# Performance work log

Measured on AMD Instinct MI355X. Metric: run time of the kernel, lower is better.

Reference implementation:

```python
import jax, jax.numpy as jnp
import numpy as np

V, DM, CD, K, CH, B, T, NC = 32000, 128, 32, 8, 4, 64, 2048, 8
LAM, RHO, LR = 0.05, 0.9, 0.03
FEAT = DM + CD + DM + DM + 2  # 418


def ln(x, w, b, eps=1e-5):
    m = x.mean(-1, keepdims=True)
    v = ((x - m) ** 2).mean(-1, keepdims=True)
    return (x - m) * jax.lax.rsqrt(v + eps) * w + b


def l2norm(x, axis):
    n = jnp.sqrt(jnp.sum(x * x, axis=axis, keepdims=True))
    return x / jnp.maximum(n, 1e-12)


def topk_shrink(x, lam, k):
    s = jnp.sign(x) * jax.nn.relu(jnp.abs(x) - lam)
    _, idx = jax.lax.top_k(jnp.abs(s), k)                      # [B,k]
    mask = jnp.any(jax.nn.one_hot(idx, s.shape[-1], dtype=bool), axis=-2)
    return jnp.where(mask, s, 0.0)


def conv1d(x, w, b, pad):
    # x [B,T,Cin], w [k,Cin,Cout]
    y = jax.lax.conv_general_dilated(x, w, (1,), ((pad, pad),),
                                     dimension_numbers=("NWC", "WIO", "NWC"))
    return y + b


def glu(x):
    a, g = jnp.split(x, 2, axis=-1)
    return a * jax.nn.sigmoid(g)


def forward(tokens, emb, in_w, in_b, c1w, c1b, c2w, c2b, op_w, op_b, on_w, on_b,
            base_D, wcu, wcc, wcdu, bcdu, wcdc, bcdc, wg, bg,
            un_w, un_b, cn_w, cn_b, cl_w, cl_b, f1w, f1b, f2w, f2b):
    token_mask = tokens != 0
    # ---- local phrase encoder ----
    x = emb[tokens]                                            # [B,T,DM]
    x = ln(x, in_w, in_b)
    y1 = glu(conv1d(x, c1w, c1b, 1))                           # [B,T,DM]
    y2 = glu(conv1d(x, c2w, c2b, 2))                           # [B,T,DM]
    y = jnp.concatenate([y1, y2], -1) @ op_w + op_b            # [B,T,DM]
    h = ln(x + y, on_w, on_b)
    # ---- surface pooling ----
    mf = token_mask.astype(h.dtype)[..., None]
    denom = jnp.maximum(mf.sum(1), 1.0)
    surface_mean = (h * mf).sum(1) / denom                     # [B,DM]
    neg = jnp.finfo(h.dtype).min
    smax = jnp.where(token_mask[..., None], h, neg).max(axis=1)
    fully = ~token_mask.any(axis=1)
    surface_max = jnp.where(fully[:, None], 0.0, smax)
    # ---- chunk mean pool ----
    chunks = T // CH
    hc = h.reshape(B, chunks, CH, DM)
    mc = token_mask.reshape(B, chunks, CH)
    mcf = mc.astype(h.dtype)
    den = jnp.maximum(mcf.sum(2, keepdims=True), 1.0)
    chunk_h = (hc * mcf[..., None]).sum(2) / den               # [B,chunks,DM]
    chunk_mask = mc.any(2)                                     # [B,chunks]
    # ---- sparse semantic field scan ----
    D0 = l2norm(jnp.broadcast_to(base_D, (B, DM, CD)), axis=1)
    c0 = jnp.zeros((B, CD), h.dtype)

    def step(carry, inp):
        D, c_prev = carry
        u, valid = inp                                         # u [B,DM], valid [B,1]
        logits = ln(u, un_w, un_b) @ wcu + ln(c_prev, cn_w, cn_b) @ wcc
        a = topk_shrink(logits, LAM, K)                        # [B,CD]
        u_hat = jnp.einsum('bdc,bc->bd', D, a)
        r = u - u_hat
        c_new = RHO * c_prev + (1.0 - RHO) * a
        c_t = valid * c_new + (1.0 - valid) * c_prev
        d_local = l2norm(D + LR * r[:, :, None] * a[:, None, :], axis=1)
        err = jnp.sqrt(jnp.sum(r * r, -1, keepdims=True))      # [B,1]
        gate = jax.nn.sigmoid(jnp.concatenate([u, c_t, err], -1) @ wg + bg)
        cand = (u @ wcdu + bcdu) + (c_t @ wcdc + bcdc)
        d_cand = l2norm(cand.reshape(B, DM, CD), axis=1)
        g = gate[:, :, None]
        d_next = l2norm((1.0 - g) * d_local + g * d_cand, axis=1)
        v = valid[:, :, None]
        d_next = v * d_next + (1.0 - v) * D
        z = jnp.einsum('bdc,bc->bd', d_next, c_t)
        return (d_next, c_t), (z, err, gate)

    xs = (chunk_h.transpose(1, 0, 2), chunk_mask.T.astype(h.dtype)[..., None])
    (Dn, c_last), (zs, errs, gates) = jax.lax.scan(step, (D0, c0), xs)
    feat = jnp.concatenate([zs[-1], c_last, surface_mean, surface_max,
                            errs[-1], gates[-1]], -1)          # [B,FEAT]
    feat = ln(feat, cl_w, cl_b)
    hcls = jax.nn.gelu(feat @ f1w + f1b, approximate=False)
    return hcls @ f2w + f2b                                    # [B,NC]


def setup_inputs() -> dict:
    ks = iter(jax.random.split(jax.random.key(0), 64))
    rn = lambda shape, s=0.02: jax.random.normal(next(ks), shape, jnp.float32) * s
    tokens = jax.random.randint(next(ks), (B, T), 0, V)
    return {
        'tokens': tokens,
        'emb': rn((V, DM)).at[0].set(0.0),
        'in_w': jnp.ones((DM,)), 'in_b': jnp.zeros((DM,)),
        'c1w': rn((3, DM, 2 * DM)), 'c1b': jnp.zeros((2 * DM,)),
        'c2w': rn((5, DM, 2 * DM)), 'c2b': jnp.zeros((2 * DM,)),
        'op_w': rn((2 * DM, DM)), 'op_b': jnp.zeros((DM,)),
        'on_w': jnp.ones((DM,)), 'on_b': jnp.zeros((DM,)),
        'base_D': rn((DM, CD)),
        'wcu': rn((DM, CD), 0.05), 'wcc': rn((CD, CD), 0.05),
        'wcdu': rn((DM, DM * CD)), 'bcdu': jnp.zeros((DM * CD,)),
        'wcdc': rn((CD, DM * CD)), 'bcdc': jnp.zeros((DM * CD,)),
        'wg': rn((DM + CD + 1, 1)), 'bg': jnp.zeros((1,)),
        'un_w': jnp.ones((DM,)), 'un_b': jnp.zeros((DM,)),
        'cn_w': jnp.ones((CD,)), 'cn_b': jnp.zeros((CD,)),
        'cl_w': jnp.ones((FEAT,)), 'cl_b': jnp.zeros((FEAT,)),
        'f1w': rn((FEAT, 2 * DM)), 'f1b': jnp.zeros((2 * DM,)),
        'f2w': rn((2 * DM, NC)), 'f2b': jnp.zeros((NC,)),
    }


def reference(tokens, emb, in_w, in_b, c1w, c1b, c2w, c2b, op_w, op_b, on_w, on_b,
              base_D, wcu, wcc, wcdu, bcdu, wcdc, bcdc, wg, bg,
              un_w, un_b, cn_w, cn_b, cl_w, cl_b, f1w, f1b, f2w, f2b):
    return forward(tokens, emb, in_w, in_b, c1w, c1b, c2w, c2b, op_w, op_b,
                   on_w, on_b, base_D, wcu, wcc, wcdu, bcdu, wcdc, bcdc, wg, bg,
                   un_w, un_b, cn_w, cn_b, cl_w, cl_b, f1w, f1b, f2w, f2b)
```

## Files before the change

### kernel.cpp

```cpp
#include <hip/hip_runtime.h>
#include <hip/hip_bf16.h>
#include <cfloat>
#include <cstdio>

#define TT   2048
#define BB   64
#define DMD  128
#define CDD  32
#define NCH  512
#define FEATN 418
#define LDW  33
#define APITCH 132
#define YPITCH 257

#define WOFF2(kc,c) ((kc)*144 + (c)*8 + (((c)>>2)<<2))

__device__ __forceinline__ float redx16(float v) {
  v += __shfl_xor(v, 1); v += __shfl_xor(v, 2);
  v += __shfl_xor(v, 4); v += __shfl_xor(v, 8);
  return v;
}
__device__ __forceinline__ float redx32(float v) { v = redx16(v); v += __shfl_xor(v, 16); return v; }
__device__ __forceinline__ float redx64(float v) { v = redx32(v); v += __shfl_xor(v, 32); return v; }
__device__ __forceinline__ float bfbits2f(unsigned int u) {
  union { unsigned int i; float f; } v; v.i = u << 16; return v.f;
}
__device__ __forceinline__ unsigned short f2bf(float f) {
  union { float f; unsigned int i; } u; u.f = f;
  unsigned int r = u.i + 0x7FFFu + ((u.i >> 16) & 1u);
  return (unsigned short)(r >> 16);
}
__device__ __forceinline__ float sigmoidf_(float x) { return 1.f / (1.f + expf(-x)); }

__device__ __forceinline__ void load_cand8(const unsigned short* cand, size_t idx, float* pf) {
  uint4 v = *reinterpret_cast<const uint4*>(cand + idx);
  pf[0] = bfbits2f(v.x & 0xFFFFu); pf[1] = bfbits2f(v.x >> 16);
  pf[2] = bfbits2f(v.y & 0xFFFFu); pf[3] = bfbits2f(v.y >> 16);
  pf[4] = bfbits2f(v.z & 0xFFFFu); pf[5] = bfbits2f(v.z >> 16);
  pf[6] = bfbits2f(v.w & 0xFFFFu); pf[7] = bfbits2f(v.w >> 16);
}

typedef __attribute__((ext_vector_type(8))) short s8v;
typedef __attribute__((ext_vector_type(4))) float f4v;
union F8 { s8v v; unsigned short u[8]; uint4 q; };

__global__ __launch_bounds__(256) void k_prep_conv(
    const float* __restrict__ c1w, const float* __restrict__ c2w,
    unsigned short* __restrict__ W3hi, unsigned short* __restrict__ W3lo,
    unsigned short* __restrict__ W5hi, unsigned short* __restrict__ W5lo) {
  int tid = blockIdx.x * 256 + threadIdx.x;
  const float* src; unsigned short *dh, *dl; int fid;
  if (tid < 12288) { fid = tid;        src = c1w; dh = W3hi; dl = W3lo; }
  else             { fid = tid - 12288; src = c2w; dh = W5hi; dl = W5lo; }
  int lane = fid & 63;
  int nt   = (fid >> 6) & 15;
  int kc   = (fid >> 10) & 3;
  int tap  = fid >> 12;
  int col  = nt * 16 + (lane & 15);
  int kb   = tap * 128 + kc * 32 + (lane >> 4) * 8;
  F8 hi, lo;
  #pragma unroll
  for (int j = 0; j < 8; ++j) {
    float wv = src[(size_t)(kb + j) * 256 + col];
    unsigned short h = f2bf(wv);
    hi.u[j] = h;
    lo.u[j] = f2bf(wv - bfbits2f(h));
  }
  *reinterpret_cast<uint4*>(dh + (size_t)fid * 8) = hi.q;
  *reinterpret_cast<uint4*>(dl + (size_t)fid * 8) = lo.q;
}

__global__ __launch_bounds__(256) void k_front(
    const int* __restrict__ tokens, const float* __restrict__ emb,
    const float* __restrict__ inw, const float* __restrict__ inb,
    const unsigned short* __restrict__ W3hi, const unsigned short* __restrict__ W3lo,
    const unsigned short* __restrict__ W5hi, const unsigned short* __restrict__ W5lo,
    const float* __restrict__ c1b, const float* __restrict__ c2b,
    const float* __restrict__ opw, const float* __restrict__ opb,
    const float* __restrict__ onw, const float* __restrict__ onb,
    const float* __restrict__ unw, const float* __restrict__ unb,
    const float* __restrict__ wcu, const float* __restrict__ wgv,
    float* __restrict__ chunk_h, float* __restrict__ validf,
    float* __restrict__ lgu, float* __restrict__ gu,
    float* __restrict__ spsum, float* __restrict__ spmax, float* __restrict__ spcnt) {
  __shared__ float A[36 * APITCH];
  __shared__ float Y[32 * YPITCH];
  __shared__ float ABf[4608];
  __shared__ float tokm[32];
  unsigned short* Ahi = (unsigned short*)ABf;
  unsigned short* Alo = Ahi + 36 * 128;
  const int b = blockIdx.y, tile = blockIdx.x;
  const int t0 = tile * 32;
  const int t = threadIdx.x;
  const int lane = t & 63, wq = t >> 6;

  for (int r = wq; r < 36; r += 4) {
    int p = t0 + r - 2;
    float2 o = make_float2(0.f, 0.f);
    if (p >= 0 && p < TT) {
      int tok = tokens[b * TT + p];
      if (lane == 0 && r >= 2 && r < 34) tokm[r - 2] = (tok != 0) ? 1.f : 0.f;
      float2 e = *reinterpret_cast<const float2*>(emb + (size_t)tok * DMD + lane * 2);
      float mean = redx64(e.x + e.y) * (1.f / 128.f);
      float d0 = e.x - mean, d1 = e.y - mean;
      float vvv = redx64(d0 * d0 + d1 * d1) * (1.f / 128.f);
      float rs = rsqrtf(vvv + 1e-5f);
      o.x = d0 * rs * inw[lane * 2]     + inb[lane * 2];
      o.y = d1 * rs * inw[lane * 2 + 1] + inb[lane * 2 + 1];
    }
    *reinterpret_cast<float2*>(&A[r * APITCH + lane * 2]) = o;
    unsigned short hx = f2bf(o.x), hy = f2bf(o.y);
    unsigned short lx = f2bf(o.x - bfbits2f(hx)), ly = f2bf(o.y - bfbits2f(hy));
    int slot = (lane >> 2) ^ (r & 7);
    int ui = r * 64 + slot * 4 + (lane & 3);
    ((unsigned int*)Ahi)[ui] = (unsigned int)hx | ((unsigned int)hy << 16);
    ((unsigned int*)Alo)[ui] = (unsigned int)lx | ((unsigned int)ly << 16);
  }
  __syncthreads();

  const int l16 = lane & 15, lk = lane >> 4;
  f4v acc3[2][4], acc5[2][4];
  #pragma unroll
  for (int mt = 0; mt < 2; ++mt)
    #pragma unroll
    for (int nf = 0; nf < 4; ++nf) { acc3[mt][nf] = (f4v)(0.f); acc5[mt][nf] = (f4v)(0.f); }
  #pragma unroll
  for (int d = 0; d < 5; ++d) {
    #pragma unroll
    for (int kc = 0; kc < 4; ++kc) {
      F8 ahi[2], alo[2];
      #pragma unroll
      for (int mt = 0; mt < 2; ++mt) {
        int arow = mt * 16 + l16 + d;
        int s = (kc * 4 + lk) ^ (arow & 7);
        ahi[mt].q = *reinterpret_cast<const uint4*>(Ahi + arow * 128 + s * 8);
        alo[mt].q = *reinterpret_cast<const uint4*>(Alo + arow * 128 + s * 8);
      }
      #pragma unroll
      for (int nf = 0; nf < 4; ++nf) {
        int nt = (nf < 2) ? (wq * 2 + nf) : (8 + wq * 2 + nf - 2);
        size_t off = ((size_t)((d * 4 + kc) * 16 + nt) * 64 + lane) * 8;
        F8 bh, bl;
        bh.q = *reinterpret_cast<const uint4*>(W5hi + off);
        bl.q = *reinterpret_cast<const uint4*>(W5lo + off);
        #pragma unroll
        for (int mt = 0; mt < 2; ++mt) {
          acc5[mt][nf] = __builtin_amdgcn_mfma_f32_16x16x32_bf16(ahi[mt].v, bh.v, acc5[mt][nf], 0, 0, 0);
          acc5[mt][nf] = __builtin_amdgcn_mfma_f32_16x16x32_bf16(ahi[mt].v, bl.v, acc5[mt][nf], 0, 0, 0);
          acc5[mt][nf] = __builtin_amdgcn_mfma_f32_16x16x32_bf16(alo[mt].v, bh.v, acc5[mt][nf], 0, 0, 0);
          acc5[mt][nf] = __builtin_amdgcn_mfma_f32_16x16x32_bf16(alo[mt].v, bl.v, acc5[mt][nf], 0, 0, 0);
        }
      }
      if (d >= 1 && d <= 3) {
        int tap = d - 1;
        #pragma unroll
        for (int nf = 0; nf < 4; ++nf) {
          int nt = (nf < 2) ? (wq * 2 + nf) : (8 + wq * 2 + nf - 2);
          size_t off = ((size_t)((tap * 4 + kc) * 16 + nt) * 64 + lane) * 8;
          F8 bh, bl;
          bh.q = *reinterpret_cast<const uint4*>(W3hi + off);
          bl.q = *reinterpret_cast<const uint4*>(W3lo + off);
          #pragma unroll
          for (int mt = 0; mt < 2; ++mt) {
            acc3[mt][nf] = __builtin_amdgcn_mfma_f32_16x16x32_bf16(ahi[mt].v, bh.v, acc3[mt][nf], 0, 0, 0);
            acc3[mt][nf] = __builtin_amdgcn_mfma_f32_16x16x32_bf16(ahi[mt].v, bl.v, acc3[mt][nf], 0, 0, 0);
            acc3[mt][nf] = __builtin_amdgcn_mfma_f32_16x16x32_bf16(alo[mt].v, bh.v, acc3[mt][nf], 0, 0, 0);
            acc3[mt][nf] = __builtin_amdgcn_mfma_f32_16x16x32_bf16(alo[mt].v, bl.v, acc3[mt][nf], 0, 0, 0);
          }
        }
      }
    }
  }
  #pragma unroll
  for (int mt = 0; mt < 2; ++mt)
    #pragma unroll
    for (int nf = 0; nf < 2; ++nf) {
      int col = wq * 32 + nf * 16 + l16;
      #pragma unroll
      for (int r = 0; r < 4; ++r) {
        int row = mt * 16 + lk * 4 + r;
        float av3 = acc3[mt][nf][r]     + c1b[col];
        float gv3 = acc3[mt][nf + 2][r] + c1b[128 + col];
        Y[row * YPITCH + col] = av3 * sigmoidf_(gv3);
        float av5 = acc5[mt][nf][r]     + c2b[col];
        float gv5 = acc5[mt][nf + 2][r] + c2b[128 + col];
        Y[row * YPITCH + 128 + col] = av5 * sigmoidf_(gv5);
      }
    }
  __syncthreads();

  const int tm = t >> 4, tn = t & 15;
  const int r0 = tm * 2;
  float* Wl = ABf;
  float acc2[2][8] = {};
  {
    const int kcw = t >> 4, cw2 = t & 15;
    {
      float4 wr0 = *reinterpret_cast<const float4*>(&opw[(size_t)kcw * 128 + cw2 * 8]);
      float4 wr1 = *reinterpret_cast<const float4*>(&opw[(size_t)kcw * 128 + cw2 * 8 + 4]);
      *reinterpret_cast<float4*>(&Wl[WOFF2(kcw, cw2)])     = wr0;
      *reinterpret_cast<float4*>(&Wl[WOFF2(kcw, cw2) + 4]) = wr1;
    }
    __syncthreads();
    for (int k0 = 0; k0 < 256; k0 += 16) {
      float* Wb = Wl + (((k0 >> 4) & 1) ? 2304 : 0);
      const bool more = (k0 + 16) < 256;
      float4 nr0, nr1;
      if (more) {
        nr0 = *reinterpret_cast<const float4*>(&opw[(size_t)(k0 + 16 + kcw) * 128 + cw2 * 8]);
        nr1 = *reinterpret_cast<const float4*>(&opw[(size_t)(k0 + 16 + kcw) * 128 + cw2 * 8 + 4]);
      }
      #pragma unroll
      for (int kc = 0; kc < 16; ++kc) {
        int k = k0 + kc;
        float y0 = Y[r0 * YPITCH + k];
        float y1 = Y[(r0 + 1) * YPITCH + k];
        float w8[8];
        *reinterpret_cast<float4*>(&w8[0]) = *reinterpret_cast<float4*>(&Wb[WOFF2(kc, tn)]);
        *reinterpret_cast<float4*>(&w8[4]) = *reinterpret_cast<float4*>(&Wb[WOFF2(kc, tn) + 4]);
        #pragma unroll
        for (int q = 0; q < 8; ++q) { acc2[0][q] += y0 * w8[q]; acc2[1][q] += y1 * w8[q]; }
      }
      if (more) {
        float* Wn = Wl + ((((k0 >> 4) + 1) & 1) ? 2304 : 0);
        *reinterpret_cast<float4*>(&Wn[WOFF2(kcw, cw2)])     = nr0;
        *reinterpret_cast<float4*>(&Wn[WOFF2(kcw, cw2) + 4]) = nr1;
      }
      __syncthreads();
    }
  }

  const int col = tn * 8;
  float hreg[2][8];
  float msk[2];
  #pragma unroll
  for (int m = 0; m < 2; ++m) {
    int row = r0 + m;
    float vals[8]; float s = 0.f;
    const float* xr = &A[(row + 2) * APITCH + col];
    #pragma unroll
    for (int q = 0; q < 8; ++q) { vals[q] = acc2[m][q] + opb[col + q] + xr[q]; s += vals[q]; }
    s = redx16(s);
    float mean = s * (1.f / 128.f);
    float vv2 = 0.f;
    #pragma unroll
    for (int q = 0; q < 8; ++q) { float d = vals[q] - mean; vv2 += d * d; }
    vv2 = redx16(vv2) * (1.f / 128.f);
    float rs = rsqrtf(vv2 + 1e-5f);
    #pragma unroll
    for (int q = 0; q < 8; ++q) hreg[m][q] = (vals[q] - mean) * rs * onw[col + q] + onb[col + q];
    msk[m] = tokm[row];
  }

  __syncthreads();
  float* partS = Y;
  float* partM = Y + 2048;
  float* lnus  = Y + 4096;
  float ps[8], pm[8];
  #pragma unroll
  for (int q = 0; q < 8; ++q) {
    ps[q] = msk[0] * hreg[0][q] + msk[1] * hreg[1][q];
    float m0 = (msk[0] != 0.f) ? hreg[0][q] : -FLT_MAX;
    float m1 = (msk[1] != 0.f) ? hreg[1][q] : -FLT_MAX;
    pm[q] = fmaxf(m0, m1);
  }
  #pragma unroll
  for (int q = 0; q < 8; ++q) { partS[tm * 128 + col + q] = ps[q]; partM[tm * 128 + col + q] = pm[q]; }

  float ccnt = msk[0] + msk[1];
  float csum[8];
  #pragma unroll
  for (int q = 0; q < 8; ++q) csum[q] = ps[q];
  #pragma unroll
  for (int q = 0; q < 8; ++q) csum[q] += __shfl_xor(csum[q], 16);
  ccnt += __shfl_xor(ccnt, 16);

  if ((tm & 1) == 0) {
    int jg = tile * 8 + (tm >> 1);
    float inv = 1.f / fmaxf(ccnt, 1.f);
    float cm[8];
    #pragma unroll
    for (int q = 0; q < 8; ++q) cm[q] = csum[q] * inv;
    *reinterpret_cast<float4*>(&chunk_h[((size_t)b * NCH + jg) * DMD + col])     = *reinterpret_cast<float4*>(&cm[0]);
    *reinterpret_cast<float4*>(&chunk_h[((size_t)b * NCH + jg) * DMD + col + 4]) = *reinterpret_cast<float4*>(&cm[4]);
    if (tn == 0) validf[jg * BB + b] = (ccnt > 0.f) ? 1.f : 0.f;
    float gp = 0.f;
    #pragma unroll
    for (int q = 0; q < 8; ++q) gp += cm[q] * wgv[col + q];
    gp = redx16(gp);
    if (tn == 0) gu[(size_t)jg * BB + b] = gp;
    float s2 = 0.f;
    #pragma unroll
    for (int q = 0; q < 8; ++q) s2 += cm[q];
    s2 = redx16(s2);
    float mean2 = s2 * (1.f / 128.f);
    float v3 = 0.f;
    #pragma unroll
    for (int q = 0; q < 8; ++q) { float d = cm[q] - mean2; v3 += d * d; }
    v3 = redx16(v3) * (1.f / 128.f);
    float rs2 = rsqrtf(v3 + 1e-5f);
    int ch = tm >> 1;
    #pragma unroll
    for (int q = 0; q < 8; ++q) lnus[ch * 128 + col + q] = (cm[q] - mean2) * rs2 * unw[col + q] + unb[col + q];
  }
  __syncthreads();
  {
    int ch = t >> 5, o = t & 31;
    float accl = 0.f;
    for (int d = 0; d < 128; ++d) accl += lnus[ch * 128 + d] * wcu[d * 32 + o];
    int jg2 = tile * 8 + ch;
    lgu[((size_t)jg2 * BB + b) * 32 + o] = accl;
  }
  if (t < 128) {
    float s3 = 0.f, m3 = -FLT_MAX;
    #pragma unroll
    for (int g = 0; g < 16; ++g) { s3 += partS[g * 128 + t]; m3 = fmaxf(m3, partM[g * 128 + t]); }
    spsum[((size_t)b * 64 + tile) * DMD + t] = s3;
    spmax[((size_t)b * 64 + tile) * DMD + t] = m3;
  }
  if (t == 128) {
    float cnt = 0.f;
    for (int r = 0; r < 32; ++r) cnt += tokm[r];
    spcnt[b * 64 + tile] = cnt;
  }
}

__global__ __launch_bounds__(128) void k_surface(
    const float* __restrict__ spsum, const float* __restrict__ spmax, const float* __restrict__ spcnt,
    float* __restrict__ smean, float* __restrict__ smax) {
  const int b = blockIdx.x, d = threadIdx.x;
  float s = 0.f, m = -FLT_MAX, cnt = 0.f;
  for (int p = 0; p < 64; ++p) {
    s += spsum[((size_t)b * 64 + p) * DMD + d];
    m = fmaxf(m, spmax[((size_t)b * 64 + p) * DMD + d]);
    cnt += spcnt[b * 64 + p];
  }
  smean[b * DMD + d] = s / fmaxf(cnt, 1.f);
  smax[b * DMD + d] = (cnt > 0.f) ? m : 0.f;
}

__global__ __launch_bounds__(256) void k_prep_w(
    const float* __restrict__ wcdu, const float* __restrict__ wcdc,
    unsigned short* __restrict__ Whi, unsigned short* __restrict__ Wlo) {
  int tid = blockIdx.x * 256 + threadIdx.x;
  int lane = tid & 63;
  int ks = (tid >> 6) % 5;
  int nt = tid / 320;
  int col = nt * 16 + (lane & 15);
  int kbase = ks * 32 + (lane >> 4) * 8;
  F8 hi, lo;
  #pragma unroll
  for (int j = 0; j < 8; ++j) {
    int k = kbase + j;
    float wv = (k < 128) ? wcdu[(size_t)k * 4096 + col] : wcdc[(size_t)(k - 128) * 4096 + col];
    unsigned short h = f2bf(wv);
    hi.u[j] = h;
    lo.u[j] = f2bf(wv - bfbits2f(h));
  }
  *reinterpret_cast<uint4*>(Whi + (size_t)tid * 8) = hi.q;
  *reinterpret_cast<uint4*>(Wlo + (size_t)tid * 8) = lo.q;
}

__global__ __launch_bounds__(256) void k_cand_mfma(
    const float* __restrict__ chunk_h, const float* __restrict__ c_g,
    const unsigned short* __restrict__ Whi, const unsigned short* __restrict__ Wlo,
    const float* __restrict__ bcdu, const float* __restrict__ bcdc,
    unsigned short* __restrict__ cand, int j0) {
  const int lj = blockIdx.y, j = j0 + lj;
  const int w = threadIdx.x >> 6, l = threadIdx.x & 63;
  const int nb = blockIdx.x * 256 + w * 64;
  const int l16 = l & 15, lk = l >> 4;
  f4v acc[4][4];
  #pragma unroll
  for (int mf = 0; mf < 4; ++mf)
    #pragma unroll
    for (int nf = 0; nf < 4; ++nf) acc[mf][nf] = (f4v)(0.f);
  #pragma unroll
  for (int ks = 0; ks < 5; ++ks) {
    F8 ahi[4], alo[4];
    #pragma unroll
    for (int mf = 0; mf < 4; ++mf) {
      int row = mf * 16 + l16;
      float av[8];
      if (ks < 4) {
        const float* src = chunk_h + ((size_t)row * NCH + j) * DMD + ks * 32 + lk * 8;
        *reinterpret_cast<float4*>(&av[0]) = *reinterpret_cast<const float4*>(src);
        *reinterpret_cast<float4*>(&av[4]) = *reinterpret_cast<const float4*>(src + 4);
      } else {
        const float* src = c_g + ((size_t)j * BB + row) * 32 + lk * 8;
        *reinterpret_cast<float4*>(&av[0]) = *reinterpret_cast<const float4*>(src);
        *reinterpret_cast<float4*>(&av[4]) = *reinterpret_cast<const float4*>(src + 4);
      }
      #pragma unroll
      for (int q = 0; q < 8; ++q) {
        unsigned short h = f2bf(av[q]);
        ahi[mf].u[q] = h;
        alo[mf].u[q] = f2bf(av[q] - bfbits2f(h));
      }
    }
    #pragma unroll
    for (int nf = 0; nf < 4; ++nf) {
      int nt = (nb >> 4) + nf;
      size_t off = (((size_t)nt * 5 + ks) * 64 + l) * 8;
      F8 bhi, blo;
      bhi.q = *reinterpret_cast<const uint4*>(Whi + off);
      blo.q = *reinterpret_cast<const uint4*>(Wlo + off);
      #pragma unroll
      for (int mf = 0; mf < 4; ++mf) {
        acc[mf][nf] = __builtin_amdgcn_mfma_f32_16x16x32_bf16(ahi[mf].v, bhi.v, acc[mf][nf], 0, 0, 0);
        acc[mf][nf] = __builtin_amdgcn_mfma_f32_16x16x32_bf16(ahi[mf].v, blo.v, acc[mf][nf], 0, 0, 0);
        acc[mf][nf] = __builtin_amdgcn_mfma_f32_16x16x32_bf16(alo[mf].v, bhi.v, acc[mf][nf], 0, 0, 0);
      }
    }
  }
  #pragma unroll
  for (int nf = 0; nf < 4; ++nf) {
    int colc = nb + nf * 16 + l16;
    float bias = bcdu[colc] + bcdc[colc];
    #pragma unroll
    for (int mf = 0; mf < 4; ++mf) {
      #pragma unroll
      for (int r = 0; r < 4; ++r) {
        int row = mf * 16 + lk * 4 + r;
        cand[((size_t)lj * BB + row) * 4096 + colc] = f2bf(acc[mf][nf][r] + bias);
      }
    }
  }
}

__global__ __launch_bounds__(64) void k_accrec(
    const float* __restrict__ lgu, const float* __restrict__ gu,
    const float* __restrict__ validf,
    const float* __restrict__ wcc, const float* __restrict__ cnw, const float* __restrict__ cnb,
    const float* __restrict__ wg, const float* __restrict__ bg,
    float* __restrict__ a_g, float* __restrict__ c_g, float* __restrict__ gpart_g) {
  __shared__ float wcc_l[CDD * CDD];
  __shared__ float cn_s[CDD];
  __shared__ float as_s[CDD];
  const int t = threadIdx.x, l = t & 31;
  const int b = blockIdx.x;
  for (int i = t; i < CDD * CDD; i += 64) wcc_l[i] = wcc[i];
  __syncthreads();
  const float cw = cnw[l], cb = cnb[l], wgc = wg[DMD + l];
  const float bgs = bg[0];
  float c = 0.f;
  float lg = lgu[(size_t)b * 32 + l];
  float vld = validf[b];
  float guv = gu[b];
  for (int j = 0; j < NCH; ++j) {
    const int jn = (j + 1 < NCH) ? j + 1 : j;
    const size_t jbn = (size_t)jn * BB + b;
    float lgN = lgu[jbn * 32 + l];
    float vldN = validf[jbn];
    float guvN = gu[jbn];
    float mean = redx32(c) * (1.f / 32.f);
    float dv = c - mean;
    float var = redx32(dv * dv) * (1.f / 32.f);
    float cn = dv * rsqrtf(var + 1e-5f) * cw + cb;
    if (t < 32) cn_s[l] = cn;
    float l0 = lg, l1 = 0.f;
    #pragma unroll
    for (int i = 0; i < 16; ++i) {
      l0 += cn_s[i] * wcc_l[i * 32 + l];
      l1 += cn_s[i + 16] * wcc_l[(i + 16) * 32 + l];
    }
    float logit = l0 + l1;
    float sv = (logit > 0.05f) ? (logit - 0.05f) : ((logit < -0.05f) ? (logit + 0.05f) : 0.f);
    float as = fabsf(sv);
    if (t < 32) as_s[l] = as;
    int r0 = 0, r1 = 0;
    #pragma unroll
    for (int i = 0; i < 16; ++i) {
      float a0 = as_s[i], a1 = as_s[i + 16];
      r0 += (a0 > as || (a0 == as && i < l)) ? 1 : 0;
      r1 += (a1 > as || (a1 == as && (i + 16) < l)) ? 1 : 0;
    }
    float av = ((r0 + r1) < 8) ? sv : 0.f;
    float ct = (vld != 0.f) ? (0.9f * c + 0.1f * av) : c;
    c = ct;
    float dotc = redx32(ct * wgc);
    if (t < 32) {
      const size_t jb = (size_t)j * BB + b;
      a_g[jb * 32 + l] = av;
      c_g[jb * 32 + l] = ct;
      if (l == 0) gpart_g[jb] = guv + dotc + bgs;
    }
    lg = lgN; vld = vldN; guv = guvN;
  }
}

__global__ __launch_bounds__(512) void k_scan_seg(
    const float* __restrict__ chunk_h, const float* __restrict__ a_gg,
    const float* __restrict__ c_g, const float* __restrict__ gpart_g,
    const float* __restrict__ validf,
    const unsigned short* __restrict__ cand, int j0, int slen,
    const float* __restrict__ wg, const float* __restrict__ base_D,
    float* __restrict__ Dst,
    const float* __restrict__ smean, const float* __restrict__ smax,
    const float* __restrict__ clw, const float* __restrict__ clb,
    const float* __restrict__ f1w, const float* __restrict__ f1b,
    const float* __restrict__ f2w, const float* __restrict__ f2b,
    float* __restrict__ out) {
  __shared__ float Dl[DMD * LDW];
  __shared__ float Cl[DMD * LDW];
  __shared__ float a_l[CDD];
  __shared__ float r_l[DMD];
  __shared__ float red[8];
  __shared__ float feat[FEATN + 2];
  __shared__ float featn[FEATN + 2];
  __shared__ float h1[256];

  const int b = blockIdx.x;
  const int t = threadIdx.x;
  const int c = t >> 4;
  const int rg = t & 15;
  const bool doInit = (j0 == 0);
  const bool doHead = (j0 + slen >= NCH);
  const float wge = wg[160];

  if (doInit) {
    for (int i = t; i < DMD * CDD; i += 512) Dl[(i >> 5) * LDW + (i & 31)] = base_D[i];
  } else {
    for (int i = t; i < DMD * CDD; i += 512) Dl[(i >> 5) * LDW + (i & 31)] = Dst[(size_t)b * 4096 + i];
  }
  __syncthreads();
  float Dv[8];
  if (doInit) {
    float s = 0.f;
    #pragma unroll
    for (int m = 0; m < 8; ++m) { Dv[m] = Dl[(rg + 16 * m) * LDW + c]; s += Dv[m] * Dv[m]; }
    s = redx16(s);
    float inv = 1.f / fmaxf(sqrtf(s), 1e-12f);
    #pragma unroll
    for (int m = 0; m < 8; ++m) { Dv[m] *= inv; Dl[(rg + 16 * m) * LDW + c] = Dv[m]; }
  } else {
    #pragma unroll
    for (int m = 0; m < 8; ++m) Dv[m] = Dl[(rg + 16 * m) * LDW + c];
  }
  float pf[8];
  load_cand8(cand, ((size_t)0 * BB + b) * 4096 + (size_t)t * 8, pf);
  float un_r = (t < DMD) ? chunk_h[((size_t)b * NCH + j0) * DMD + t] : 0.f;
  float a_col = a_gg[((size_t)j0 * BB + b) * 32 + c];
  if (t < 32) a_l[t] = a_gg[((size_t)j0 * BB + b) * 32 + t];
  float gpart = gpart_g[(size_t)j0 * BB + b];
  float vld = validf[(size_t)j0 * BB + b];
  float err = 0.f, gate = 0.f;

  for (int lj = 0; lj < slen; ++lj) {
    __syncthreads();
    {
      int dd = t >> 2, cc0 = (t & 3) * 8;
      #pragma unroll
      for (int q = 0; q < 8; ++q) Cl[dd * LDW + cc0 + q] = pf[q];
    }
    if (t < DMD) {
      float uh = 0.f;
      #pragma unroll
      for (int cc = 0; cc < 32; ++cc) uh += a_l[cc] * Dl[t * LDW + cc];
      float rr = un_r - uh;
      r_l[t] = rr;
      float rp = redx64(rr * rr);
      if ((t & 63) == 0) red[t >> 6] = rp;
    }
    __syncthreads();
    err = sqrtf(red[0] + red[1]);
    gate = sigmoidf_(gpart + err * wge);
    const int ljn = (lj + 1 < slen) ? (lj + 1) : lj;
    const int jn = j0 + ljn;
    float pfN[8];
    load_cand8(cand, ((size_t)ljn * BB + b) * 4096 + (size_t)t * 8, pfN);
    float unN = (t < DMD) ? chunk_h[((size_t)b * NCH + jn) * DMD + t] : 0.f;
    float aColN = a_gg[((size_t)jn * BB + b) * 32 + c];
    float a32N = (t < 32) ? a_gg[((size_t)jn * BB + b) * 32 + t] : 0.f;
    float gpN = gpart_g[(size_t)jn * BB + b];
    float vldN = validf[(size_t)jn * BB + b];
    float dl[8], dcv[8], dn[8];
    float sl = 0.f, sc = 0.f;
    #pragma unroll
    for (int m = 0; m < 8; ++m) {
      int e = (rg + 16 * m) * LDW + c;
      dl[m] = Dv[m] + 0.03f * r_l[rg + 16 * m] * a_col;
      sl += dl[m] * dl[m];
      dcv[m] = Cl[e];
      sc += dcv[m] * dcv[m];
    }
    sl = redx16(sl); sc = redx16(sc);
    float il = 1.f / fmaxf(sqrtf(sl), 1e-12f);
    float ic = 1.f / fmaxf(sqrtf(sc), 1e-12f);
    float g1 = 1.f - gate;
    float sn = 0.f;
    #pragma unroll
    for (int m = 0; m < 8; ++m) { dn[m] = g1 * dl[m] * il + gate * dcv[m] * ic; sn += dn[m] * dn[m]; }
    sn = redx16(sn);
    float inn = 1.f / fmaxf(sqrtf(sn), 1e-12f);
    const bool vb = (vld != 0.f);
    #pragma unroll
    for (int m = 0; m < 8; ++m) {
      if (vb) Dv[m] = dn[m] * inn;
      Dl[(rg + 16 * m) * LDW + c] = Dv[m];
    }
    if (t < 32) a_l[t] = a32N;
    #pragma unroll
    for (int q = 0; q < 8; ++q) pf[q] = pfN[q];
    un_r = unN; a_col = aColN; gpart = gpN; vld = vldN;
  }
  __syncthreads();
  for (int i = t; i < 4096; i += 512) Dst[(size_t)b * 4096 + i] = Dl[(i >> 5) * LDW + (i & 31)];
  if (!doHead) return;
  if (t < 32) a_l[t] = c_g[((size_t)(NCH - 1) * BB + b) * 32 + t];
  __syncthreads();
  if (t < DMD) {
    float z = 0.f;
    #pragma unroll
    for (int cc = 0; cc < 32; ++cc) z += Dl[t * LDW + cc] * a_l[cc];
    feat[t] = z;
    feat[160 + t] = smean[b * DMD + t];
    feat[288 + t] = smax[b * DMD + t];
  }
  if (t >= 128 && t < 160) feat[t] = a_l[t - 128];
  if (t == 0) { feat[416] = err; feat[417] = gate; }
  __syncthreads();
  float fv = (t < FEATN) ? feat[t] : 0.f;
  float ws1 = redx64(fv);
  if ((t & 63) == 0) red[t >> 6] = ws1;
  __syncthreads();
  float tot = 0.f;
  #pragma unroll
  for (int w = 0; w < 8; ++w) tot += red[w];
  float mean = tot * (1.f / 418.f);
  float dvv = (t < FEATN) ? (fv - mean) : 0.f;
  float ws2 = redx64(dvv * dvv);
  __syncthreads();
  if ((t & 63) == 0) red[t >> 6] = ws2;
  __syncthreads();
  float vtot = 0.f;
  #pragma unroll
  for (int w = 0; w < 8; ++w) vtot += red[w];
  float rs = rsqrtf(vtot * (1.f / 418.f) + 1e-5f);
  if (t < FEATN) featn[t] = (fv - mean) * rs * clw[t] + clb[t];
  __syncthreads();
  if (t < 256) {
    float acc = f1b[t];
    for (int f = 0; f < FEATN; ++f) acc += featn[f] * f1w[(size_t)f * 256 + t];
    h1[t] = acc * 0.5f * (1.f + erff(acc * 0.70710678f));
  }
  __syncthreads();
  if (t < 8) {
    float acc = f2b[t];
    #pragma unroll 8
    for (int i = 0; i < 256; ++i) acc += h1[i] * f2w[i * 8 + t];
    out[b * 8 + t] = acc;
  }
}

extern "C" void kernel_launch(void* const* d_in, const int* in_sizes, int n_in,
                              void* d_out, int out_size, void* d_ws, size_t ws_size,
                              hipStream_t stream) {
  const int*   tokens = (const int*)d_in[0];
  const float* emb    = (const float*)d_in[1];
  const float* in_w   = (const float*)d_in[2];
  const float* in_b   = (const float*)d_in[3];
  const float* c1w    = (const float*)d_in[4];
  const float* c1b    = (const float*)d_in[5];
  const float* c2w    = (const float*)d_in[6];
  const float* c2b    = (const float*)d_in[7];
  const float* op_w   = (const float*)d_in[8];
  const float* op_b   = (const float*)d_in[9];
  const float* on_w   = (const float*)d_in[10];
  const float* on_b   = (const float*)d_in[11];
  const float* base_D = (const float*)d_in[12];
  const float* wcu    = (const float*)d_in[13];
  const float* wcc    = (const float*)d_in[14];
  const float* wcdu   = (const float*)d_in[15];
  const float* bcdu   = (const float*)d_in[16];
  const float* wcdc   = (const float*)d_in[17];
  const float* bcdc   = (const float*)d_in[18];
  const float* wg     = (const float*)d_in[19];
  const float* bg     = (const float*)d_in[20];
  const float* un_w   = (const float*)d_in[21];
  const float* un_b   = (const float*)d_in[22];
  const float* cn_w   = (const float*)d_in[23];
  const float* cn_b   = (const float*)d_in[24];
  const float* cl_w   = (const float*)d_in[25];
  const float* cl_b   = (const float*)d_in[26];
  const float* f1w    = (const float*)d_in[27];
  const float* f1b    = (const float*)d_in[28];
  const float* f2w    = (const float*)d_in[29];
  const float* f2b    = (const float*)d_in[30];

  const size_t CHEL = (size_t)BB * NCH * DMD;
  const size_t NB   = (size_t)NCH * BB;
  size_t fixedFloats = CHEL + NB + NB * 32 + NB
                     + (size_t)BB * 64 * DMD * 2 + (size_t)BB * 64
                     + (size_t)BB * DMD * 2 + (size_t)BB * 4096
                     + NB * 32 + NB * 32 + NB;
  const size_t WFRAG  = 655360ull;
  const size_t W3FR   = 98304ull;
  const size_t W5FR   = 163840ull;
  const size_t WSWZ_BYTES = (2ull * WFRAG + 2ull * W3FR + 2ull * W5FR) * 2ull;
  const size_t FIXED_BYTES = fixedFloats * 4 + WSWZ_BYTES;
  const size_t SEG_UNIT = (size_t)BB * 4096 * 2;
  int S = 512;
  while (S > 1 && (size_t)S * SEG_UNIT + FIXED_BYTES > ws_size) S >>= 1;

  unsigned short* cand = (unsigned short*)d_ws;
  unsigned short* Whi  = (unsigned short*)((char*)d_ws + (size_t)S * SEG_UNIT);
  unsigned short* Wlo  = Whi + WFRAG;
  unsigned short* W3hi = Wlo + WFRAG;
  unsigned short* W3lo = W3hi + W3FR;
  unsigned short* W5hi = W3lo + W3FR;
  unsigned short* W5lo = W5hi + W5FR;
  float* base = (float*)(W5lo + W5FR);
  float* chunk_h = base; base += CHEL;
  float* validf  = base; base += NB;
  float* lgu     = base; base += NB * 32;
  float* gu      = base; base += NB;
  float* spsum   = base; base += (size_t)BB * 64 * DMD;
  float* spmax   = base; base += (size_t)BB * 64 * DMD;
  float* spcnt   = base; base += (size_t)BB * 64;
  float* smean   = base; base += (size_t)BB * DMD;
  float* smaxv   = base; base += (size_t)BB * DMD;
  float* Dst     = base; base += (size_t)BB * 4096;
  float* a_g     = base; base += NB * 32;
  float* c_g     = base; base += NB * 32;
  float* gpart   = base; base += NB;
  float* out = (float*)d_out;
  fprintf(stderr, "[hsfc69] ws_size=%zu fixed=%zu S=%d total=%zu\n",
          ws_size, FIXED_BYTES, S, FIXED_BYTES + (size_t)S * SEG_UNIT);

  k_prep_w<<<dim3(320), dim3(256), 0, stream>>>(wcdu, wcdc, Whi, Wlo);
  k_prep_conv<<<dim3(128), dim3(256), 0, stream>>>(c1w, c2w, W3hi, W3lo, W5hi, W5lo);
  k_front<<<dim3(64, BB), dim3(256), 0, stream>>>(
      tokens, emb, in_w, in_b, W3hi, W3lo, W5hi, W5lo, c1b, c2b,
      op_w, op_b, on_w, on_b, un_w, un_b, wcu, wg,
      chunk_h, validf, lgu, gu, spsum, spmax, spcnt);
  k_surface<<<dim3(BB), dim3(128), 0, stream>>>(spsum, spmax, spcnt, smean, smaxv);
  k_accrec<<<dim3(BB), dim3(64), 0, stream>>>(
      lgu, gu, validf, wcc, cn_w, cn_b, wg, bg, a_g, c_g, gpart);
  for (int j0 = 0; j0 < NCH; j0 += S) {
    k_cand_mfma<<<dim3(16, S), dim3(256), 0, stream>>>(
        chunk_h, c_g, Whi, Wlo, bcdu, bcdc, cand, j0);
    k_scan_seg<<<dim3(BB), dim3(512), 0, stream>>>(
        chunk_h, a_g, c_g, gpart, validf, cand, j0, S,
        wg, base_D, Dst, smean, smaxv, cl_w, cl_b, f1w, f1b, f2w, f2b, out);
  }
}
```

Before: 2.995 ms.

## Store candidate dictionaries column-major so scan threads read own columns directly

```diff
diff --git a/kernel.cpp b/kernel.cpp
--- a/kernel.cpp
+++ b/kernel.cpp
@@ -9,11 +9,12 @@
 #define CDD  32
 #define NCH  512
 #define FEATN 418
-#define LDW  33
 #define APITCH 132
 #define YPITCH 257
 
 #define WOFF2(kc,c) ((kc)*144 + (c)*8 + (((c)>>2)<<2))
+
+#define DSWZ(c,dd) ((((((c)>>2) + (dd) + ((dd)>>3)) & 7) << 2) + ((c)&3))
 
 __device__ __forceinline__ float redx16(float v) {
   v += __shfl_xor(v, 1); v += __shfl_xor(v, 2);
@@ -343,16 +344,18 @@
     const float* __restrict__ wcdu, const float* __restrict__ wcdc,
     unsigned short* __restrict__ Whi, unsigned short* __restrict__ Wlo) {
   int tid = blockIdx.x * 256 + threadIdx.x;
-  int lane = tid & 63;
-  int ks = (tid >> 6) % 5;
-  int nt = tid / 320;
-  int col = nt * 16 + (lane & 15);
-  int kbase = ks * 32 + (lane >> 4) * 8;
+  int l = tid & 63;
+  int f = tid >> 6;
+  int ks = f % 5;
+  int ddt = (f / 5) & 7;
+  int c = f / 40;
+  int colc = (ddt * 16 + (l & 15)) * 32 + c;
+  int kbase = ks * 32 + (l >> 4) * 8;
   F8 hi, lo;
   #pragma unroll
   for (int j = 0; j < 8; ++j) {
     int k = kbase + j;
-    float wv = (k < 128) ? wcdu[(size_t)k * 4096 + col] : wcdc[(size_t)(k - 128) * 4096 + col];
+    float wv = (k < 128) ? wcdu[(size_t)k * 4096 + colc] : wcdc[(size_t)(k - 128) * 4096 + colc];
     unsigned short h = f2bf(wv);
     hi.u[j] = h;
     lo.u[j] = f2bf(wv - bfbits2f(h));
@@ -366,9 +369,12 @@
     const unsigned short* __restrict__ Whi, const unsigned short* __restrict__ Wlo,
     const float* __restrict__ bcdu, const float* __restrict__ bcdc,
     unsigned short* __restrict__ cand, int j0) {
+  __shared__ unsigned short stg[4 * 64 * 72];
   const int lj = blockIdx.y, j = j0 + lj;
+  const int bx = blockIdx.x;
   const int w = threadIdx.x >> 6, l = threadIdx.x & 63;
-  const int nb = blockIdx.x * 256 + w * 64;
+  const int c = bx * 2 + (w & 1);
+  const int ddw = (w >> 1) * 64;
   const int l16 = l & 15, lk = l >> 4;
   f4v acc[4][4];
   #pragma unroll
@@ -400,8 +406,8 @@
     }
     #pragma unroll
     for (int nf = 0; nf < 4; ++nf) {
-      int nt = (nb >> 4) + nf;
-      size_t off = (((size_t)nt * 5 + ks) * 64 + l) * 8;
+      int ddt = (ddw >> 4) + nf;
+      size_t off = (((size_t)(c * 8 + ddt) * 5 + ks) * 64 + l) * 8;
       F8 bhi, blo;
       bhi.q = *reinterpret_cast<const uint4*>(Whi + off);
       blo.q = *reinterpret_cast<const uint4*>(Wlo + off);
@@ -415,16 +421,30 @@
   }
   #pragma unroll
   for (int nf = 0; nf < 4; ++nf) {
-    int colc = nb + nf * 16 + l16;
+    int dd = ddw + nf * 16 + l16;
+    int colc = dd * 32 + c;
     float bias = bcdu[colc] + bcdc[colc];
     #pragma unroll
     for (int mf = 0; mf < 4; ++mf) {
       #pragma unroll
       for (int r = 0; r < 4; ++r) {
-        int row = mf * 16 + lk * 4 + r;
-        cand[((size_t)lj * BB + row) * 4096 + colc] = f2bf(acc[mf][nf][r] + bias);
-      }
-    }
+        int bb2 = mf * 16 + lk * 4 + r;
+        stg[w * 4608 + bb2 * 72 + nf * 16 + l16] = f2bf(acc[mf][nf][r] + bias);
+      }
+    }
+  }
+  __syncthreads();
+  #pragma unroll
+  for (int k = 0; k < 8; ++k) {
+    int cid = k * 256 + threadIdx.x;
+    int rw = cid >> 9;
+    int rem = cid & 511;
+    int bb2 = rem >> 3;
+    int dd0 = (rem & 7) * 8;
+    int c_r = bx * 2 + (rw & 1);
+    int ddb = (rw >> 1) * 64;
+    uint4 v = *reinterpret_cast<const uint4*>(&stg[rw * 4608 + bb2 * 72 + dd0]);
+    *reinterpret_cast<uint4*>(&cand[((size_t)lj * BB + bb2) * 4096 + c_r * 128 + ddb + dd0]) = v;
   }
 }
 
@@ -501,8 +521,7 @@
     const float* __restrict__ f1w, const float* __restrict__ f1b,
     const float* __restrict__ f2w, const float* __restrict__ f2b,
     float* __restrict__ out) {
-  __shared__ float Dl[DMD * LDW];
-  __shared__ float Cl[DMD * LDW];
+  __shared__ float Dl[DMD * 32];
   __shared__ float a_l[CDD];
   __shared__ float r_l[DMD];
   __shared__ float red[8];
@@ -513,32 +532,34 @@
   const int b = blockIdx.x;
   const int t = threadIdx.x;
   const int c = t >> 4;
-  const int rg = t & 15;
+  const int rb = t & 15;
   const bool doInit = (j0 == 0);
   const bool doHead = (j0 + slen >= NCH);
   const float wge = wg[160];
 
-  if (doInit) {
-    for (int i = t; i < DMD * CDD; i += 512) Dl[(i >> 5) * LDW + (i & 31)] = base_D[i];
-  } else {
-    for (int i = t; i < DMD * CDD; i += 512) Dl[(i >> 5) * LDW + (i & 31)] = Dst[(size_t)b * 4096 + i];
-  }
-  __syncthreads();
   float Dv[8];
+  #pragma unroll
+  for (int i = 0; i < 8; ++i) {
+    int dd = rb * 8 + i;
+    Dv[i] = doInit ? base_D[dd * 32 + c] : Dst[(size_t)b * 4096 + dd * 32 + c];
+  }
   if (doInit) {
     float s = 0.f;
     #pragma unroll
-    for (int m = 0; m < 8; ++m) { Dv[m] = Dl[(rg + 16 * m) * LDW + c]; s += Dv[m] * Dv[m]; }
+    for (int i = 0; i < 8; ++i) s += Dv[i] * Dv[i];
     s = redx16(s);
     float inv = 1.f / fmaxf(sqrtf(s), 1e-12f);
     #pragma unroll
-    for (int m = 0; m < 8; ++m) { Dv[m] *= inv; Dl[(rg + 16 * m) * LDW + c] = Dv[m]; }
-  } else {
-    #pragma unroll
-    for (int m = 0; m < 8; ++m) Dv[m] = Dl[(rg + 16 * m) * LDW + c];
-  }
+    for (int i = 0; i < 8; ++i) Dv[i] *= inv;
+  }
+  #pragma unroll
+  for (int i = 0; i < 8; ++i) {
+    int dd = rb * 8 + i;
+    Dl[dd * 32 + DSWZ(c, dd)] = Dv[i];
+  }
+
   float pf[8];
-  load_cand8(cand, ((size_t)0 * BB + b) * 4096 + (size_t)t * 8, pf);
+  load_cand8(cand, ((size_t)0 * BB + b) * 4096 + (size_t)c * 128 + rb * 8, pf);
   float un_r = (t < DMD) ? chunk_h[((size_t)b * NCH + j0) * DMD + t] : 0.f;
   float a_col = a_gg[((size_t)j0 * BB + b) * 32 + c];
   if (t < 32) a_l[t] = a_gg[((size_t)j0 * BB + b) * 32 + t];
@@ -548,15 +569,16 @@
 
   for (int lj = 0; lj < slen; ++lj) {
     __syncthreads();
-    {
-      int dd = t >> 2, cc0 = (t & 3) * 8;
-      #pragma unroll
-      for (int q = 0; q < 8; ++q) Cl[dd * LDW + cc0 + q] = pf[q];
-    }
     if (t < DMD) {
+      const int r = t;
       float uh = 0.f;
       #pragma unroll
-      for (int cc = 0; cc < 32; ++cc) uh += a_l[cc] * Dl[t * LDW + cc];
+      for (int qs = 0; qs < 8; ++qs) {
+        int sq = (qs + r + (r >> 3)) & 7;
+        float4 d4 = *reinterpret_cast<float4*>(&Dl[r * 32 + sq * 4]);
+        uh += a_l[qs * 4 + 0] * d4.x + a_l[qs * 4 + 1] * d4.y
+            + a_l[qs * 4 + 2] * d4.z + a_l[qs * 4 + 3] * d4.w;
+      }
       float rr = un_r - uh;
       r_l[t] = rr;
       float rp = redx64(rr * rr);
@@ -568,21 +590,22 @@
     const int ljn = (lj + 1 < slen) ? (lj + 1) : lj;
     const int jn = j0 + ljn;
     float pfN[8];
-    load_cand8(cand, ((size_t)ljn * BB + b) * 4096 + (size_t)t * 8, pfN);
+    load_cand8(cand, ((size_t)ljn * BB + b) * 4096 + (size_t)c * 128 + rb * 8, pfN);
     float unN = (t < DMD) ? chunk_h[((size_t)b * NCH + jn) * DMD + t] : 0.f;
     float aColN = a_gg[((size_t)jn * BB + b) * 32 + c];
     float a32N = (t < 32) ? a_gg[((size_t)jn * BB + b) * 32 + t] : 0.f;
     float gpN = gpart_g[(size_t)jn * BB + b];
     float vldN = validf[(size_t)jn * BB + b];
-    float dl[8], dcv[8], dn[8];
+    float rr8[8];
+    *reinterpret_cast<float4*>(&rr8[0]) = *reinterpret_cast<float4*>(&r_l[rb * 8]);
+    *reinterpret_cast<float4*>(&rr8[4]) = *reinterpret_cast<float4*>(&r_l[rb * 8 + 4]);
+    float dl[8], dn[8];
     float sl = 0.f, sc = 0.f;
     #pragma unroll
-    for (int m = 0; m < 8; ++m) {
-      int e = (rg + 16 * m) * LDW + c;
-      dl[m] = Dv[m] + 0.03f * r_l[rg + 16 * m] * a_col;
-      sl += dl[m] * dl[m];
-      dcv[m] = Cl[e];
-      sc += dcv[m] * dcv[m];
+    for (int i = 0; i < 8; ++i) {
+      dl[i] = Dv[i] + 0.03f * rr8[i] * a_col;
+      sl += dl[i] * dl[i];
+      sc += pf[i] * pf[i];
     }
     sl = redx16(sl); sc = redx16(sc);
     float il = 1.f / fmaxf(sqrtf(sl), 1e-12f);
@@ -590,14 +613,15 @@
     float g1 = 1.f - gate;
     float sn = 0.f;
     #pragma unroll
-    for (int m = 0; m < 8; ++m) { dn[m] = g1 * dl[m] * il + gate * dcv[m] * ic; sn += dn[m] * dn[m]; }
+    for (int i = 0; i < 8; ++i) { dn[i] = g1 * dl[i] * il + gate * pf[i] * ic; sn += dn[i] * dn[i]; }
     sn = redx16(sn);
     float inn = 1.f / fmaxf(sqrtf(sn), 1e-12f);
     const bool vb = (vld != 0.f);
     #pragma unroll
-    for (int m = 0; m < 8; ++m) {
-      if (vb) Dv[m] = dn[m] * inn;
-      Dl[(rg + 16 * m) * LDW + c] = Dv[m];
+    for (int i = 0; i < 8; ++i) {
+      if (vb) Dv[i] = dn[i] * inn;
+      int dd = rb * 8 + i;
+      Dl[dd * 32 + DSWZ(c, dd)] = Dv[i];
     }
     if (t < 32) a_l[t] = a32N;
     #pragma unroll
@@ -605,14 +629,22 @@
     un_r = unN; a_col = aColN; gpart = gpN; vld = vldN;
   }
   __syncthreads();
-  for (int i = t; i < 4096; i += 512) Dst[(size_t)b * 4096 + i] = Dl[(i >> 5) * LDW + (i & 31)];
+  #pragma unroll
+  for (int i = 0; i < 8; ++i)
+    Dst[(size_t)b * 4096 + (rb * 8 + i) * 32 + c] = Dv[i];
   if (!doHead) return;
   if (t < 32) a_l[t] = c_g[((size_t)(NCH - 1) * BB + b) * 32 + t];
   __syncthreads();
   if (t < DMD) {
+    const int r = t;
     float z = 0.f;
     #pragma unroll
-    for (int cc = 0; cc < 32; ++cc) z += Dl[t * LDW + cc] * a_l[cc];
+    for (int qs = 0; qs < 8; ++qs) {
+      int sq = (qs + r + (r >> 3)) & 7;
+      float4 d4 = *reinterpret_cast<float4*>(&Dl[r * 32 + sq * 4]);
+      z += a_l[qs * 4 + 0] * d4.x + a_l[qs * 4 + 1] * d4.y
+         + a_l[qs * 4 + 2] * d4.z + a_l[qs * 4 + 3] * d4.w;
+    }
     feat[t] = z;
     feat[160 + t] = smean[b * DMD + t];
     feat[288 + t] = smax[b * DMD + t];
```

After: 2.937 ms. About the same (-1.9%).
